# Kernel tuning notes

Measured on AMD Instinct MI355X. Metric: run time of the kernel, lower is better.

The kernel has to match this reference:

```python
import jax, jax.numpy as jnp
import numpy as np

NUM_LAYERS = 3
N = 4096
DIM = 512
TOPK = 8
BIG = 1.0e9
EPS_COS = 1e-8
EPS_NORM = 1e-12
BN_EPS = 1e-5
LAM_K = 64.0
LAM_Z = 16.0
SIGMA_INTRA = 0.99
ALPHA = np.linspace(1.0, 1.2, NUM_LAYERS)
BETA = np.linspace(0.0, 0.0, NUM_LAYERS)


def setup_inputs() -> dict:
    key = jax.random.key(0)
    ks = jax.random.split(key, 6)
    feats = jax.random.normal(ks[0], (NUM_LAYERS, N, DIM), dtype=jnp.float32)
    labels = jax.random.randint(ks[1], (N,), 0, 64, dtype=jnp.int64)
    fc1_w = jax.random.normal(ks[2], (NUM_LAYERS, DIM, DIM), dtype=jnp.float32) * (1.0 / np.sqrt(DIM))
    fc2_w = jax.random.normal(ks[3], (NUM_LAYERS, DIM, DIM), dtype=jnp.float32) * (1.0 / np.sqrt(DIM))
    bn_gamma = jnp.ones((NUM_LAYERS, DIM), dtype=jnp.float32)
    bn_beta = jnp.zeros((NUM_LAYERS, DIM), dtype=jnp.float32)
    proj_w = jax.random.normal(ks[4], (768, DIM), dtype=jnp.float32) * (1.0 / np.sqrt(DIM))
    return {"feats": feats, "labels": labels, "fc1_w": fc1_w, "fc2_w": fc2_w,
            "bn_gamma": bn_gamma, "bn_beta": bn_beta, "proj_w": proj_w}


def _l2norm(x, axis=-1):
    return x / jnp.maximum(jnp.linalg.norm(x, axis=axis, keepdims=True), EPS_NORM)


def _pairwise_cosine(G):
    Gn = _l2norm(G)
    sim = Gn @ Gn.T
    return jnp.clip(sim, -1.0 + EPS_COS, 1.0 - EPS_COS)


def _knn_mask(sim, base_mask, topk):
    n = sim.shape[0]
    masked = (sim - BIG * jnp.eye(n, dtype=sim.dtype)) * base_mask - (1.0 - base_mask) * BIG
    k = min(topk, max(n - 1, 1))
    idx = jax.lax.top_k(masked, k)[1]  # [N, k]
    st = jnp.zeros_like(sim).at[jnp.arange(n)[:, None], idx].set(1.0)
    return jnp.maximum(st, st.T)


def _build_intra_inter(sim, labels, topk):
    same = (labels[None, :] == labels[:, None]).astype(sim.dtype)
    diff = 1.0 - same
    m_intra = _knn_mask(sim, same, topk)
    m_inter = _knn_mask(sim, diff, topk)
    sim_intra = jnp.maximum(sim * m_intra, 0.0)
    sim_inter = jnp.maximum(sim * m_inter, 0.0)
    return sim_intra, sim_inter


def _normalize_sym(sim_graph, eps=1e-8):
    d = jnp.maximum(sim_graph.sum(axis=1), eps)
    dinv = d ** -0.5
    return dinv[:, None] * sim_graph * dinv[None, :]  # == diag(dinv) @ S @ diag(dinv)


def _diffusion(K, t_diff=1):
    out = K
    for _ in range(max(t_diff - 1, 0)):
        out = out @ K
    return out


def _bn_train(x, gamma, beta):
    m = x.mean(axis=0)
    v = x.var(axis=0)  # biased, as torch BN training
    return (x - m) / jnp.sqrt(v + BN_EPS) * gamma + beta


def _gam(S, G, w1, w2, gamma, beta):
    Z = S @ (G @ w1.T)
    Z = jax.nn.relu(_bn_train(Z, gamma, beta))
    Z = S @ (Z @ w2.T)
    return Z + G


def reference(feats, labels, fc1_w, fc2_w, bn_gamma, bn_beta, proj_w):
    n = feats.shape[1]
    eye = jnp.eye(n, dtype=feats.dtype)
    same = (labels[None, :] == labels[:, None]).astype(feats.dtype)

    K_list, Z_list = [], []
    for i in range(NUM_LAYERS):
        G = feats[i]
        sim = _pairwise_cosine(G)
        sim_intra, sim_inter = _build_intra_inter(sim, labels, TOPK)
        sim_graph = float(ALPHA[i]) * sim_intra + float(BETA[i]) * sim_inter + 1e-6 * eye
        S = _normalize_sym(sim_graph)
        K = _diffusion(S, t_diff=1)
        Z = _gam(S, G, fc1_w[i], fc2_w[i], bn_gamma[i], bn_beta[i])
        K_list.append(K)
        Z_list.append(Z)

    loss_K = jnp.zeros((), dtype=feats.dtype)
    loss_Z = jnp.zeros((), dtype=feats.dtype)
    for i in range(1, NUM_LAYERS):
        K_tgt = jax.lax.stop_gradient(K_list[i])
        loss_K = loss_K + jnp.mean((K_list[i - 1] - K_tgt) ** 2)
        Zp = _l2norm(Z_list[i - 1] @ proj_w.T)
        Zc = _l2norm(Z_list[i] @ proj_w.T)
        loss_Z = loss_Z + jnp.mean((Zp - jax.lax.stop_gradient(Zc)) ** 2)

    K_idea = _diffusion(same * SIGMA_INTRA, t_diff=1)
    loss_idea = jnp.mean((K_list[-1] - K_idea) ** 2)
    return LAM_K * loss_K + LAM_Z * loss_Z + loss_idea
```

## Files before the change

### kernel.cpp

```cpp
#include <hip/hip_runtime.h>
#include <math.h>
#include <stdint.h>

#define NROWS 4096
#define DIM   512
#define NCLS  64
#define CAP   128
#define PD    768
#define NL    3
#define PARTSZ (size_t)(NCLS * 4 * 1024)

typedef __attribute__((ext_vector_type(8))) short short8v;
typedef __attribute__((ext_vector_type(4))) float f32x4;

__device__ __forceinline__ unsigned short f2bf(float f) {
  unsigned u = __float_as_uint(f);
  unsigned r = (u + 0x7FFF + ((u >> 16) & 1)) >> 16;
  return (unsigned short)r;
}

__device__ __forceinline__ void gload_lds16(const void* g, void* l) {
  auto* lp = reinterpret_cast<__attribute__((address_space(3))) unsigned int*>(
      reinterpret_cast<uintptr_t>(l));
  const auto* gp = reinterpret_cast<const __attribute__((address_space(1))) unsigned int*>(
      reinterpret_cast<uintptr_t>(g));
  __builtin_amdgcn_global_load_lds(gp, lp, 16, 0, 0);
}

__device__ __forceinline__ float waveReduce(float v) {
#pragma unroll
  for (int o = 32; o > 0; o >>= 1) v += __shfl_down(v, o);
  return v;
}

__device__ __forceinline__ float blockReduce(float v) {
  __shared__ float sh[4];
  int lane = threadIdx.x & 63, wv = threadIdx.x >> 6;
  v = waveReduce(v);
  if (lane == 0) sh[wv] = v;
  __syncthreads();
  float t = 0.f;
  if (threadIdx.x == 0) {
    int nw = (blockDim.x + 63) >> 6;
    for (int i = 0; i < nw; ++i) t += sh[i];
  }
  return t;
}

__global__ __launch_bounds__(256) void k_hist(const int* __restrict__ labels, int* __restrict__ chunkCnt) {
  __shared__ int h[NCLS];
  int t = threadIdx.x;
  if (t < NCLS) h[t] = 0;
  __syncthreads();
  atomicAdd(&h[labels[blockIdx.x * 256 + t]], 1);
  __syncthreads();
  if (t < NCLS) chunkCnt[blockIdx.x * NCLS + t] = h[t];
}

__global__ void k_scan(const int* __restrict__ chunkCnt, int* __restrict__ cnt,
                       int* __restrict__ off, int* __restrict__ chunkBase, float* __restrict__ acc) {
  __shared__ int sc[NCLS];
  int c = threadIdx.x;
  if (c < 8) acc[c] = 0.f;
  int tot = 0;
  for (int b = 0; b < 16; ++b) tot += chunkCnt[b * NCLS + c];
  cnt[c] = tot;
  sc[c] = tot;
  __syncthreads();
  if (c == 0) {
    int s = 0;
    for (int i = 0; i < NCLS; ++i) { int tv = sc[i]; sc[i] = s; s += tv; }
  }
  __syncthreads();
  int run = sc[c];
  off[c] = run;
  for (int b = 0; b < 16; ++b) { chunkBase[b * NCLS + c] = run; run += chunkCnt[b * NCLS + c]; }
  if (c == 0) off[NCLS] = NROWS;
}

__global__ __launch_bounds__(256) void k_scatter(const int* __restrict__ labels, const int* __restrict__ chunkBase,
                                                 int* __restrict__ perm, int* __restrict__ clsp) {
  __shared__ int lab[256];
  int t = threadIdx.x;
  int r = blockIdx.x * 256 + t;
  int c = labels[r];
  lab[t] = c;
  __syncthreads();
  int rank = 0;
  for (int j = 0; j < t; ++j) rank += (lab[j] == c);
  int pos = chunkBase[blockIdx.x * NCLS + c] + rank;
  perm[pos] = r;
  clsp[pos] = c;
}

__global__ __launch_bounds__(128) void k_prepw(const float* __restrict__ feats, const int* __restrict__ perm,
                                               unsigned short* __restrict__ Gpb, float* __restrict__ invn,
                                               const float4* __restrict__ fc1, const float4* __restrict__ fc2,
                                               const float4* __restrict__ proj,
                                               ushort4* __restrict__ w1, ushort4* __restrict__ w2,
                                               ushort4* __restrict__ pj) {
  int y = blockIdx.y;
  if (y == NL) {
    const int nW = NL * DIM * DIM / 4;
    const int nP = PD * DIM / 4;
    int idx = blockIdx.x * 128 + threadIdx.x;
    const float4* src; ushort4* dst; int k;
    if (idx < nW) { src = fc1; dst = w1; k = idx; }
    else if (idx < 2 * nW) { src = fc2; dst = w2; k = idx - nW; }
    else if (idx < 2 * nW + nP) { src = proj; dst = pj; k = idx - 2 * nW; }
    else return;
    float4 v = src[k];
    ushort4 o;
    o.x = f2bf(v.x); o.y = f2bf(v.y); o.z = f2bf(v.z); o.w = f2bf(v.w);
    dst[k] = o;
    return;
  }
  __shared__ float red[2];
  int l = y;
  const float* G = feats + (size_t)l * NROWS * DIM;
  unsigned short* Gp = Gpb + (size_t)l * NROWS * DIM;
  int row = blockIdx.x, t = threadIdx.x;
  const float4* src = (const float4*)(G + (size_t)perm[row] * DIM);
  float4 v = src[t];
  ushort4 b;
  b.x = f2bf(v.x); b.y = f2bf(v.y); b.z = f2bf(v.z); b.w = f2bf(v.w);
  *(ushort4*)(Gp + (size_t)row * DIM + t * 4) = b;
  float ss = v.x * v.x + v.y * v.y + v.z * v.z + v.w * v.w;
  ss = waveReduce(ss);
  if ((t & 63) == 0) red[t >> 6] = ss;
  __syncthreads();
  if (t == 0) invn[l * NROWS + row] = 1.f / fmaxf(sqrtf(red[0] + red[1]), 1e-12f);
}

__global__ __launch_bounds__(256) void k_sim(const unsigned short* __restrict__ Gpb,
                                             const float* __restrict__ invn,
                                             const int* __restrict__ cnt, const int* __restrict__ off,
                                             float* __restrict__ sim) {
  int l = blockIdx.z;
  const unsigned short* Gp = Gpb + (size_t)l * NROWS * DIM;
  const float* inv = invn + (size_t)l * NROWS;
  float* sm = sim + (size_t)l * NCLS * CAP * CAP;
  int c = blockIdx.y;
  int n = min(cnt[c], CAP);
  int ti = blockIdx.x >> 2, tj = blockIdx.x & 3;
  if (ti * 32 >= n || tj * 32 >= n) return;
  int base = off[c];
  __shared__ short As[32][40];
  __shared__ short Bs[32][40];
  const int t = threadIdx.x;
  const int lane = t & 63, wv = t >> 6;
  const int qi = wv >> 1, qj = wv & 1;
  const int fr = lane & 15, kg = lane >> 4;
  const int half = t >> 7, tt = t & 127;
  const int srow = tt >> 2, scol = (tt & 3) * 8;
  int gr = (half ? tj : ti) * 32 + srow;
  const unsigned short* ps = Gp + (size_t)(base + min(gr, n - 1)) * DIM + scol;
  short* dst = half ? &Bs[srow][scol] : &As[srow][scol];
  f32x4 acc = {};
  for (int k0 = 0; k0 < DIM; k0 += 32) {
    short8v v = *(const short8v*)(ps + k0);
    __syncthreads();
    *(short8v*)dst = v;
    __syncthreads();
    short8v af = *(const short8v*)&As[qi * 16 + fr][kg * 8];
    short8v bf = *(const short8v*)&Bs[qj * 16 + fr][kg * 8];
    acc = __builtin_amdgcn_mfma_f32_16x16x32_bf16(af, bf, acc, 0, 0, 0);
  }
  int gj = tj * 32 + qj * 16 + fr;
  int r0 = ti * 32 + qi * 16 + kg * 4;
  if (gj < n) {
    float sj = inv[base + gj];
#pragma unroll
    for (int r = 0; r < 4; ++r) {
      int gi = r0 + r;
      if (gi < n) {
        float v = acc[r] * inv[base + gi] * sj;
        v = fminf(fmaxf(v, -1.0f + 1e-8f), 1.0f - 1e-8f);
        sm[((size_t)c * CAP + gi) * CAP + gj] = v;
      }
    }
  }
}

__global__ __launch_bounds__(256) void k_topk(const float* __restrict__ sim, const int* __restrict__ cnt,
                                              const int* __restrict__ off, const int* __restrict__ clsp,
                                              int* __restrict__ t8) {
  int l = blockIdx.y;
  const float* sm = sim + (size_t)l * NCLS * CAP * CAP;
  int* t8l = t8 + (size_t)l * NROWS * 8;
  int pr = blockIdx.x * 256 + threadIdx.x;
  if (pr >= NROWS) return;
  int c = clsp[pr];
  int n = min(cnt[c], CAP);
  int loc = pr - off[c];
  const float4* row4 = (const float4*)(sm + ((size_t)c * CAP + loc) * CAP);
  float bv[8]; int bi[8];
#pragma unroll
  for (int q = 0; q < 8; ++q) { bv[q] = -3e38f; bi[q] = -1; }
  for (int j4 = 0; j4 < CAP / 4; ++j4) {
    if (j4 * 4 >= n) break;
    float4 v4 = row4[j4];
    float vv[4] = {v4.x, v4.y, v4.z, v4.w};
#pragma unroll
    for (int k = 0; k < 4; ++k) {
      int j = j4 * 4 + k;
      if (j >= n || j == loc) continue;
      float v = vv[k];
      if (v > bv[7]) {
        bv[7] = v; bi[7] = j;
#pragma unroll
        for (int q = 7; q > 0; --q) {
          if (bv[q] > bv[q - 1]) {
            float tv = bv[q]; bv[q] = bv[q - 1]; bv[q - 1] = tv;
            int tq = bi[q]; bi[q] = bi[q - 1]; bi[q - 1] = tq;
          }
        }
      }
    }
  }
#pragma unroll
  for (int q = 0; q < 8; ++q) t8l[pr * 8 + q] = bi[q];
}

__global__ __launch_bounds__(256) void k_buildS1(const float* __restrict__ sim, const int* __restrict__ cnt,
                                                 const int* __restrict__ off, const int* __restrict__ t8,
                                                 float* __restrict__ S, float* __restrict__ dinv) {
  int l = blockIdx.z;
  float alpha = 1.0f + 0.1f * l;
  const float* sm = sim + (size_t)l * NCLS * CAP * CAP;
  float* Sl = S + (size_t)l * NCLS * CAP * CAP;
  const int* t8l = t8 + (size_t)l * NROWS * 8;
  float* dv = dinv + (size_t)l * NCLS * CAP;
  int c = blockIdx.x;
  int n = min(cnt[c], CAP);
  int i0 = blockIdx.y * 32;
  if (i0 >= n) return;
  int base = off[c];
  __shared__ int sh8[CAP * 8];
  for (int i = threadIdx.x; i < n * 8; i += 256) sh8[i] = t8l[base * 8 + i];
  __syncthreads();
  int r = threadIdx.x >> 3;
  int lj = threadIdx.x & 7;
  int i = i0 + r;
  float d = 0.f;
  if (i < n) {
    int my8[8];
#pragma unroll
    for (int q = 0; q < 8; ++q) my8[q] = sh8[i * 8 + q];
    const float* srow = sm + ((size_t)c * CAP + i) * CAP;
    float* wrow = Sl + ((size_t)c * CAP + i) * CAP;
    for (int j = lj; j < n; j += 8) {
      float w;
      if (j == i) w = 1e-6f;
      else {
        bool m = false;
#pragma unroll
        for (int q = 0; q < 8; ++q) m = m || (my8[q] == j) || (sh8[j * 8 + q] == i);
        w = m ? alpha * fmaxf(srow[j], 0.f) : 0.f;
      }
      wrow[j] = w;
      d += w;
    }
  }
  d += __shfl_xor(d, 1);
  d += __shfl_xor(d, 2);
  d += __shfl_xor(d, 4);
  if (lj == 0 && i < n) dv[c * CAP + i] = 1.f / sqrtf(fmaxf(d, 1e-8f));
}

__global__ __launch_bounds__(256) void k_buildS2(float* __restrict__ S, const float* __restrict__ dinv,
                                                 const int* __restrict__ cnt) {
  int l = blockIdx.z;
  float* Sl = S + (size_t)l * NCLS * CAP * CAP;
  const float* dv = dinv + (size_t)l * NCLS * CAP;
  int c = blockIdx.x;
  int n = min(cnt[c], CAP);
  int i0 = blockIdx.y * 32;
  if (i0 >= n) return;
  __shared__ float sd[CAP];
  for (int k = threadIdx.x; k < n; k += 256) sd[k] = dv[c * CAP + k];
  __syncthreads();
  for (int p = threadIdx.x; p < 32 * CAP; p += 256) {
    int r = p >> 7, j = p & (CAP - 1);
    int i = i0 + r;
    if (i < n && j < n)
      Sl[((size_t)c * CAP + i) * CAP + j] *= sd[i] * sd[j];
  }
}

__global__ __launch_bounds__(256) void k_gemm_bf16(const short* __restrict__ A, const short* __restrict__ B,
                                                   float* __restrict__ C, int N,
                                                   long sA, long sB, long sC) {
  int l = blockIdx.z;
  A += (size_t)l * sA; B += (size_t)l * sB; C += (size_t)l * sC;
  __shared__ __align__(16) short As[128][32];
  __shared__ __align__(16) short Bs[64][32];
  const int row0 = blockIdx.x * 128, col0 = blockIdx.y * 64;
  const int t = threadIdx.x;
  const int lane = t & 63, wv = t >> 6;
  const int fr = lane & 15, kg = lane >> 4;
  const int srow = lane >> 2, skb = (lane & 3) * 8;
  const short* pa = A + (size_t)(row0 + wv * 32 + srow) * DIM + skb;
  const short* pb = B + (size_t)(col0 + wv * 16 + srow) * DIM + skb;
  f32x4 acc[2][4] = {};
  for (int kt = 0; kt < DIM; kt += 32) {
    __syncthreads();
    gload_lds16(pa + kt, &As[wv * 32][0]);
    gload_lds16(pa + kt + (size_t)16 * DIM, &As[wv * 32 + 16][0]);
    gload_lds16(pb + kt, &Bs[wv * 16][0]);
    __syncthreads();
    short8v af[2], bf[4];
#pragma unroll
    for (int i = 0; i < 2; ++i) af[i] = *(const short8v*)&As[wv * 32 + i * 16 + fr][kg * 8];
#pragma unroll
    for (int j = 0; j < 4; ++j) bf[j] = *(const short8v*)&Bs[j * 16 + fr][kg * 8];
#pragma unroll
    for (int i = 0; i < 2; ++i)
#pragma unroll
      for (int j = 0; j < 4; ++j)
        acc[i][j] = __builtin_amdgcn_mfma_f32_16x16x32_bf16(af[i], bf[j], acc[i][j], 0, 0, 0);
  }
#pragma unroll
  for (int i = 0; i < 2; ++i) {
    int r0 = row0 + wv * 32 + i * 16 + kg * 4;
#pragma unroll
    for (int j = 0; j < 4; ++j) {
      int cc = col0 + j * 16 + fr;
#pragma unroll
      for (int r = 0; r < 4; ++r)
        C[(size_t)(r0 + r) * N + cc] = acc[i][j][r];
    }
  }
}

__global__ __launch_bounds__(256) void k_spmm4(const float* __restrict__ S, const float* __restrict__ X,
                                               const float* __restrict__ Gfeat, const int* __restrict__ perm,
                                               float* __restrict__ Y, unsigned short* __restrict__ Yb,
                                               float* __restrict__ part,
                                               const int* __restrict__ cnt, const int* __restrict__ off) {
  int l = blockIdx.z >> 2;
  int zc = blockIdx.z & 3;
  const float* Sl = S + (size_t)l * NCLS * CAP * CAP;
  const float4* X4 = (const float4*)(X + (size_t)l * NROWS * DIM);
  const float4* G4 = Gfeat ? (const float4*)(Gfeat + (size_t)l * NROWS * DIM) : (const float4*)nullptr;
  float4* Y4 = Y ? (float4*)(Y + (size_t)l * NROWS * DIM) : (float4*)nullptr;
  ushort4* Yb4 = Yb ? (ushort4*)(Yb + (size_t)l * NROWS * DIM) : (ushort4*)nullptr;
  int c = blockIdx.x;
  int n = min(cnt[c], CAP);
  int i0 = zc * 32;
  float* pslot = part ? part + (size_t)l * PARTSZ + (size_t)(c * 4 + zc) * 1024 : (float*)nullptr;
  __shared__ float sS[32][CAP];
  if (i0 >= n) {
    if (pslot) {
      int col = blockIdx.y * 256 + threadIdx.x;
      pslot[col] = 0.f;
      pslot[512 + col] = 0.f;
    }
    return;
  }
  int base = off[c];
  int lane = threadIdx.x & 63;
  int col4 = blockIdx.y * 64 + lane;
  int ty = threadIdx.x >> 6;
  for (int idx = threadIdx.x; idx < 32 * n; idx += 256) {
    int r = idx / n, j = idx - r * n;
    sS[r][j] = (i0 + r < n) ? Sl[((size_t)c * CAP + i0 + r) * CAP + j] : 0.f;
  }
  __syncthreads();
  float4 acc[8];
#pragma unroll
  for (int ii = 0; ii < 8; ++ii) acc[ii] = make_float4(0.f, 0.f, 0.f, 0.f);
  for (int j = 0; j < n; ++j) {
    float4 x = X4[(size_t)(base + j) * 128 + col4];
#pragma unroll
    for (int ii = 0; ii < 8; ++ii) {
      float s = sS[ty * 8 + ii][j];
      acc[ii].x += s * x.x;
      acc[ii].y += s * x.y;
      acc[ii].z += s * x.z;
      acc[ii].w += s * x.w;
    }
  }
  float s1[4] = {0.f, 0.f, 0.f, 0.f}, s2[4] = {0.f, 0.f, 0.f, 0.f};
#pragma unroll
  for (int ii = 0; ii < 8; ++ii) {
    int r = i0 + ty * 8 + ii;
    if (r < n) {
      size_t o = (size_t)(base + r) * 128 + col4;
      float4 v = acc[ii];
      if (G4) {
        float4 g = G4[(size_t)perm[base + r] * 128 + col4];
        v.x += g.x; v.y += g.y; v.z += g.z; v.w += g.w;
      }
      if (pslot) {
        s1[0] += v.x; s1[1] += v.y; s1[2] += v.z; s1[3] += v.w;
        s2[0] += v.x * v.x; s2[1] += v.y * v.y; s2[2] += v.z * v.z; s2[3] += v.w * v.w;
      }
      if (Yb4) {
        ushort4 ob;
        ob.x = f2bf(v.x); ob.y = f2bf(v.y); ob.z = f2bf(v.z); ob.w = f2bf(v.w);
        Yb4[o] = ob;
      } else {
        Y4[o] = v;
      }
    }
  }
  if (pslot) {
    __syncthreads();
    float* scr = &sS[0][0];
#pragma unroll
    for (int q = 0; q < 4; ++q) {
      scr[(ty * 64 + lane) * 8 + q] = s1[q];
      scr[(ty * 64 + lane) * 8 + 4 + q] = s2[q];
    }
    __syncthreads();
    if (ty == 0) {
#pragma unroll
      for (int q = 0; q < 4; ++q) {
        float a = 0.f, b = 0.f;
#pragma unroll
        for (int g = 0; g < 4; ++g) {
          a += scr[(g * 64 + lane) * 8 + q];
          b += scr[(g * 64 + lane) * 8 + 4 + q];
        }
        int col = blockIdx.y * 256 + lane * 4 + q;
        pslot[col] = a;
        pslot[512 + col] = b;
      }
    }
  }
}

__global__ __launch_bounds__(64) void k_bnfin(const float* __restrict__ part, const float* __restrict__ gamma,
                                              const float* __restrict__ beta, float* __restrict__ sc) {
  int l = blockIdx.y;
  const float* pl = part + (size_t)l * PARTSZ;
  int k = blockIdx.x * 64 + threadIdx.x;
  float s = 0.f, s2 = 0.f;
  for (int b = 0; b < NCLS * 4; ++b) {
    s += pl[b * 1024 + k];
    s2 += pl[b * 1024 + 512 + k];
  }
  float m = s * (1.f / NROWS);
  float var = s2 * (1.f / NROWS) - m * m;
  float sg = gamma[l * DIM + k] / sqrtf(var + 1e-5f);
  sc[l * 2 * DIM + k] = sg;
  sc[l * 2 * DIM + DIM + k] = beta[l * DIM + k] - m * sg;
}

__global__ __launch_bounds__(256) void k_bnrelu(const float4* __restrict__ X, const float* __restrict__ sc,
                                                ushort4* __restrict__ Yb) {
  int l = blockIdx.y;
  const float4* Xl = X + (size_t)l * (NROWS * DIM / 4);
  const float* scl = sc + (size_t)l * 2 * DIM;
  ushort4* Yl = Yb + (size_t)l * (NROWS * DIM / 4);
  int i = blockIdx.x * blockDim.x + threadIdx.x;
  int cb = (i * 4) & (DIM - 1);
  float4 v = Xl[i];
  ushort4 o;
  o.x = f2bf(fmaxf(v.x * scl[cb + 0] + scl[DIM + cb + 0], 0.f));
  o.y = f2bf(fmaxf(v.y * scl[cb + 1] + scl[DIM + cb + 1], 0.f));
  o.z = f2bf(fmaxf(v.z * scl[cb + 2] + scl[DIM + cb + 2], 0.f));
  o.w = f2bf(fmaxf(v.w * scl[cb + 3] + scl[DIM + cb + 3], 0.f));
  Yl[i] = o;
}

__global__ __launch_bounds__(192) void k_rownormP(float* __restrict__ P) {
  __shared__ float red[3];
  __shared__ float s_inv;
  int l = blockIdx.y;
  float* Pl = P + (size_t)l * NROWS * PD;
  int row = blockIdx.x, t = threadIdx.x;
  float4* p = (float4*)(Pl + (size_t)row * PD);
  float4 v = p[t];
  float ss = v.x * v.x + v.y * v.y + v.z * v.z + v.w * v.w;
  ss = waveReduce(ss);
  if ((t & 63) == 0) red[t >> 6] = ss;
  __syncthreads();
  if (t == 0) s_inv = 1.f / fmaxf(sqrtf(red[0] + red[1] + red[2]), 1e-12f);
  __syncthreads();
  float inv = s_inv;
  v.x *= inv; v.y *= inv; v.z *= inv; v.w *= inv;
  p[t] = v;
}

__global__ __launch_bounds__(256) void k_loss(const float* __restrict__ S, const float* __restrict__ P,
                                              const int* __restrict__ cnt,
                                              float target, float cK, float cI, float cZ,
                                              float* __restrict__ acc) {
  int y = blockIdx.y;
  if (y < 3) {
    if (blockIdx.x >= NCLS) return;
    const float* Sa = S + (size_t)y * NCLS * CAP * CAP;
    const float* Sb = nullptr;
    float coef;
    if (y < 2) { Sb = Sa + (size_t)NCLS * CAP * CAP; coef = cK; }
    else { Sa = S + (size_t)2 * NCLS * CAP * CAP; coef = cI; }
    int c = blockIdx.x;
    int n = min(cnt[c], CAP);
    float s = 0.f;
    for (int p = threadIdx.x; p < CAP * CAP; p += 256) {
      int i = p >> 7, j = p & (CAP - 1);
      if (i < n && j < n) {
        size_t o = ((size_t)c * CAP + i) * CAP + j;
        float d = Sb ? (Sa[o] - Sb[o]) : (Sa[o] - target);
        s += d * d;
      }
    }
    s = blockReduce(s);
    if (threadIdx.x == 0) atomicAdd(acc, s * coef);
  } else {
    int yy = y - 3;
    const float* A = P + (size_t)yy * NROWS * PD;
    const float* B = A + (size_t)NROWS * PD;
    const int nel = NROWS * PD;
    float s = 0.f;
    for (int i = blockIdx.x * blockDim.x + threadIdx.x; i < nel; i += gridDim.x * blockDim.x) {
      float d = A[i] - B[i];
      s += d * d;
    }
    s = blockReduce(s);
    if (threadIdx.x == 0) atomicAdd(acc, s * cZ);
  }
}

__global__ void k_final(const float* __restrict__ acc, float* __restrict__ out) {
  if (threadIdx.x == 0) out[0] = acc[0];
}

extern "C" void kernel_launch(void* const* d_in, const int* in_sizes, int n_in,
                              void* d_out, int out_size, void* d_ws, size_t ws_size,
                              hipStream_t stream) {
  const float* feats = (const float*)d_in[0];
  const int* labels = (const int*)d_in[1];
  const float* fc1 = (const float*)d_in[2];
  const float* fc2 = (const float*)d_in[3];
  const float* gamma = (const float*)d_in[4];
  const float* beta = (const float*)d_in[5];
  const float* proj = (const float*)d_in[6];
  float* out = (float*)d_out;

  char* w = (char*)d_ws;
  auto alloc = [&](size_t bytes) { char* p = w; w += (bytes + 255) & ~(size_t)255; return p; };
  float* bufA = (float*)alloc((size_t)NL * NROWS * DIM * 4);
  float* bufB = (float*)alloc((size_t)NL * NROWS * DIM * 4);
  unsigned short* Gpb = (unsigned short*)alloc((size_t)NL * NROWS * DIM * 2);
  unsigned short* actb = (unsigned short*)alloc((size_t)NL * NROWS * DIM * 2);
  unsigned short* W1b = (unsigned short*)alloc((size_t)NL * DIM * DIM * 2);
  unsigned short* W2b = (unsigned short*)alloc((size_t)NL * DIM * DIM * 2);
  unsigned short* Pjb = (unsigned short*)alloc((size_t)PD * DIM * 2);
  float* sim  = (float*)alloc((size_t)NL * NCLS * CAP * CAP * 4);
  float* S    = (float*)alloc((size_t)NL * NCLS * CAP * CAP * 4);
  float* P    = (float*)alloc((size_t)NL * NROWS * PD * 4);
  float* invn = (float*)alloc((size_t)NL * NROWS * 4);
  float* dinv = (float*)alloc((size_t)NL * NCLS * CAP * 4);
  float* part = (float*)alloc((size_t)NL * PARTSZ * 4);
  float* bnsc = (float*)alloc((size_t)NL * 2 * DIM * 4);
  float* acc  = (float*)alloc(256);
  int* cnt  = (int*)alloc(NCLS * 4);
  int* offc = (int*)alloc((NCLS + 1) * 4);
  int* perm = (int*)alloc(NROWS * 4);
  int* clsp = (int*)alloc(NROWS * 4);
  int* t8   = (int*)alloc((size_t)NL * NROWS * 8 * 4);
  int* chunkCnt  = (int*)alloc(16 * NCLS * 4);
  int* chunkBase = (int*)alloc(16 * NCLS * 4);

  const float LAM_K = 64.f, LAM_Z = 16.f, SIGMA = 0.99f;
  const float cK = LAM_K / ((float)NROWS * (float)NROWS);
  const float cZ = LAM_Z / ((float)NROWS * (float)PD);
  const float cI = 1.f / ((float)NROWS * (float)NROWS);
  const long sAct = (long)NROWS * DIM;
  const long sW = (long)DIM * DIM;

  hipLaunchKernelGGL(k_hist, dim3(16), dim3(256), 0, stream, labels, chunkCnt);
  hipLaunchKernelGGL(k_scan, dim3(1), dim3(64), 0, stream, chunkCnt, cnt, offc, chunkBase, acc);
  hipLaunchKernelGGL(k_scatter, dim3(16), dim3(256), 0, stream, labels, chunkBase, perm, clsp);

  hipLaunchKernelGGL(k_prepw, dim3(NROWS, NL + 1), dim3(128), 0, stream, feats, perm, Gpb, invn,
                     (const float4*)fc1, (const float4*)fc2, (const float4*)proj,
                     (ushort4*)W1b, (ushort4*)W2b, (ushort4*)Pjb);

  hipLaunchKernelGGL(k_sim, dim3(16, NCLS, NL), dim3(256), 0, stream, Gpb, invn, cnt, offc, sim);
  hipLaunchKernelGGL(k_topk, dim3(NROWS / 256, NL), dim3(256), 0, stream, sim, cnt, offc, clsp, t8);
  hipLaunchKernelGGL(k_buildS1, dim3(NCLS, CAP / 32, NL), dim3(256), 0, stream, sim, cnt, offc, t8, S, dinv);
  hipLaunchKernelGGL(k_buildS2, dim3(NCLS, CAP / 32, NL), dim3(256), 0, stream, S, dinv, cnt);

  hipLaunchKernelGGL(k_gemm_bf16, dim3(NROWS / 128, DIM / 64, NL), dim3(256), 0, stream,
                     (const short*)Gpb, (const short*)W1b, bufA, DIM, sAct, sW, (long)NROWS * DIM);
  hipLaunchKernelGGL(k_spmm4, dim3(NCLS, DIM / 256, 4 * NL), dim3(256), 0, stream, S, bufA,
                     (const float*)nullptr, (const int*)nullptr, bufB, (unsigned short*)nullptr, part, cnt, offc);
  hipLaunchKernelGGL(k_bnfin, dim3(DIM / 64, NL), dim3(64), 0, stream, part, gamma, beta, bnsc);
  hipLaunchKernelGGL(k_bnrelu, dim3(NROWS * DIM / 4 / 256, NL), dim3(256), 0, stream,
                     (const float4*)bufB, bnsc, (ushort4*)actb);
  hipLaunchKernelGGL(k_gemm_bf16, dim3(NROWS / 128, DIM / 64, NL), dim3(256), 0, stream,
                     (const short*)actb, (const short*)W2b, bufB, DIM, sAct, sW, (long)NROWS * DIM);
  hipLaunchKernelGGL(k_spmm4, dim3(NCLS, DIM / 256, 4 * NL), dim3(256), 0, stream, S, bufB,
                     feats, perm, (float*)nullptr, actb, (float*)nullptr, cnt, offc);
  hipLaunchKernelGGL(k_gemm_bf16, dim3(NROWS / 128, PD / 64, NL), dim3(256), 0, stream,
                     (const short*)actb, (const short*)Pjb, P, PD, sAct, 0L, (long)NROWS * PD);
  hipLaunchKernelGGL(k_rownormP, dim3(NROWS, NL), dim3(192), 0, stream, P);

  hipLaunchKernelGGL(k_loss, dim3(512, 5), dim3(256), 0, stream, S, P, cnt, SIGMA, cK, cI, cZ, acc);

  hipLaunchKernelGGL(k_final, dim3(1), dim3(64), 0, stream, acc, out);
}
```

Measured before the change: 265.2 us.

## Fuse projection row norms into GEMM epilogue and widen SpMM row tiles

The projection GEMM epilogue now accumulates per-row sums of squares with shuffles and atomics into a buffer zeroed in the prep kernel. That removes the separate row-normalization pass over P, and the loss kernel applies the inverse norms on the fly. Separately, the SpMM kernel now handles 64 rows per block instead of 32, halving the number of blocks and BN partial slots. The cost is more register pressure (16 float4 accumulators), a larger shared-memory tile, less parallelism, and atomic contention on the row-norm buffer.

New measurement: 262.9 us. Within noise of the previous version (-0.9%).

```diff
diff --git a/kernel.cpp b/kernel.cpp
--- a/kernel.cpp
+++ b/kernel.cpp
@@ -8,7 +8,7 @@
 #define CAP   128
 #define PD    768
 #define NL    3
-#define PARTSZ (size_t)(NCLS * 4 * 1024)
+#define PARTSZ (size_t)(NCLS * 2 * 1024)
 
 typedef __attribute__((ext_vector_type(8))) short short8v;
 typedef __attribute__((ext_vector_type(4))) float f32x4;
@@ -98,7 +98,7 @@
                                                const float4* __restrict__ fc1, const float4* __restrict__ fc2,
                                                const float4* __restrict__ proj,
                                                ushort4* __restrict__ w1, ushort4* __restrict__ w2,
-                                               ushort4* __restrict__ pj) {
+                                               ushort4* __restrict__ pj, float* __restrict__ rnorm) {
   int y = blockIdx.y;
   if (y == NL) {
     const int nW = NL * DIM * DIM / 4;
@@ -108,7 +108,11 @@
     if (idx < nW) { src = fc1; dst = w1; k = idx; }
     else if (idx < 2 * nW) { src = fc2; dst = w2; k = idx - nW; }
     else if (idx < 2 * nW + nP) { src = proj; dst = pj; k = idx - 2 * nW; }
-    else return;
+    else {
+      int z = idx - (2 * nW + nP);
+      if (z < NL * NROWS) rnorm[z] = 0.f;
+      return;
+    }
     float4 v = src[k];
     ushort4 o;
     o.x = f2bf(v.x); o.y = f2bf(v.y); o.z = f2bf(v.z); o.w = f2bf(v.w);
@@ -289,10 +293,11 @@
 }
 
 __global__ __launch_bounds__(256) void k_gemm_bf16(const short* __restrict__ A, const short* __restrict__ B,
-                                                   float* __restrict__ C, int N,
+                                                   float* __restrict__ C, float* __restrict__ rnorm, int N,
                                                    long sA, long sB, long sC) {
   int l = blockIdx.z;
   A += (size_t)l * sA; B += (size_t)l * sB; C += (size_t)l * sC;
+  if (rnorm) rnorm += (size_t)l * NROWS;
   __shared__ __align__(16) short As[128][32];
   __shared__ __align__(16) short Bs[64][32];
   const int row0 = blockIdx.x * 128, col0 = blockIdx.y * 64;
@@ -330,16 +335,28 @@
       for (int r = 0; r < 4; ++r)
         C[(size_t)(r0 + r) * N + cc] = acc[i][j][r];
     }
-  }
-}
-
-__global__ __launch_bounds__(256) void k_spmm4(const float* __restrict__ S, const float* __restrict__ X,
-                                               const float* __restrict__ Gfeat, const int* __restrict__ perm,
-                                               float* __restrict__ Y, unsigned short* __restrict__ Yb,
-                                               float* __restrict__ part,
-                                               const int* __restrict__ cnt, const int* __restrict__ off) {
-  int l = blockIdx.z >> 2;
-  int zc = blockIdx.z & 3;
+    if (rnorm) {
+#pragma unroll
+      for (int r = 0; r < 4; ++r) {
+        float ss = acc[i][0][r] * acc[i][0][r] + acc[i][1][r] * acc[i][1][r] +
+                   acc[i][2][r] * acc[i][2][r] + acc[i][3][r] * acc[i][3][r];
+        ss += __shfl_xor(ss, 1);
+        ss += __shfl_xor(ss, 2);
+        ss += __shfl_xor(ss, 4);
+        ss += __shfl_xor(ss, 8);
+        if (fr == 0) atomicAdd(&rnorm[r0 + r], ss);
+      }
+    }
+  }
+}
+
+__global__ __launch_bounds__(256) void k_spmm64(const float* __restrict__ S, const float* __restrict__ X,
+                                                const float* __restrict__ Gfeat, const int* __restrict__ perm,
+                                                float* __restrict__ Y, unsigned short* __restrict__ Yb,
+                                                float* __restrict__ part,
+                                                const int* __restrict__ cnt, const int* __restrict__ off) {
+  int l = blockIdx.z >> 1;
+  int zc = blockIdx.z & 1;
   const float* Sl = S + (size_t)l * NCLS * CAP * CAP;
   const float4* X4 = (const float4*)(X + (size_t)l * NROWS * DIM);
   const float4* G4 = Gfeat ? (const float4*)(Gfeat + (size_t)l * NROWS * DIM) : (const float4*)nullptr;
@@ -347,9 +364,9 @@
   ushort4* Yb4 = Yb ? (ushort4*)(Yb + (size_t)l * NROWS * DIM) : (ushort4*)nullptr;
   int c = blockIdx.x;
   int n = min(cnt[c], CAP);
-  int i0 = zc * 32;
-  float* pslot = part ? part + (size_t)l * PARTSZ + (size_t)(c * 4 + zc) * 1024 : (float*)nullptr;
-  __shared__ float sS[32][CAP];
+  int i0 = zc * 64;
+  float* pslot = part ? part + (size_t)l * PARTSZ + (size_t)(c * 2 + zc) * 1024 : (float*)nullptr;
+  __shared__ float sS[64][CAP];
   if (i0 >= n) {
     if (pslot) {
       int col = blockIdx.y * 256 + threadIdx.x;
@@ -362,19 +379,19 @@
   int lane = threadIdx.x & 63;
   int col4 = blockIdx.y * 64 + lane;
   int ty = threadIdx.x >> 6;
-  for (int idx = threadIdx.x; idx < 32 * n; idx += 256) {
+  for (int idx = threadIdx.x; idx < 64 * n; idx += 256) {
     int r = idx / n, j = idx - r * n;
     sS[r][j] = (i0 + r < n) ? Sl[((size_t)c * CAP + i0 + r) * CAP + j] : 0.f;
   }
   __syncthreads();
-  float4 acc[8];
-#pragma unroll
-  for (int ii = 0; ii < 8; ++ii) acc[ii] = make_float4(0.f, 0.f, 0.f, 0.f);
+  float4 acc[16];
+#pragma unroll
+  for (int ii = 0; ii < 16; ++ii) acc[ii] = make_float4(0.f, 0.f, 0.f, 0.f);
   for (int j = 0; j < n; ++j) {
     float4 x = X4[(size_t)(base + j) * 128 + col4];
 #pragma unroll
-    for (int ii = 0; ii < 8; ++ii) {
-      float s = sS[ty * 8 + ii][j];
+    for (int ii = 0; ii < 16; ++ii) {
+      float s = sS[ty * 16 + ii][j];
       acc[ii].x += s * x.x;
       acc[ii].y += s * x.y;
       acc[ii].z += s * x.z;
@@ -383,8 +400,8 @@
   }
   float s1[4] = {0.f, 0.f, 0.f, 0.f}, s2[4] = {0.f, 0.f, 0.f, 0.f};
 #pragma unroll
-  for (int ii = 0; ii < 8; ++ii) {
-    int r = i0 + ty * 8 + ii;
+  for (int ii = 0; ii < 16; ++ii) {
+    int r = i0 + ty * 16 + ii;
     if (r < n) {
       size_t o = (size_t)(base + r) * 128 + col4;
       float4 v = acc[ii];
@@ -437,7 +454,7 @@
   const float* pl = part + (size_t)l * PARTSZ;
   int k = blockIdx.x * 64 + threadIdx.x;
   float s = 0.f, s2 = 0.f;
-  for (int b = 0; b < NCLS * 4; ++b) {
+  for (int b = 0; b < NCLS * 2; ++b) {
     s += pl[b * 1024 + k];
     s2 += pl[b * 1024 + 512 + k];
   }
@@ -465,27 +482,8 @@
   Yl[i] = o;
 }
 
-__global__ __launch_bounds__(192) void k_rownormP(float* __restrict__ P) {
-  __shared__ float red[3];
-  __shared__ float s_inv;
-  int l = blockIdx.y;
-  float* Pl = P + (size_t)l * NROWS * PD;
-  int row = blockIdx.x, t = threadIdx.x;
-  float4* p = (float4*)(Pl + (size_t)row * PD);
-  float4 v = p[t];
-  float ss = v.x * v.x + v.y * v.y + v.z * v.z + v.w * v.w;
-  ss = waveReduce(ss);
-  if ((t & 63) == 0) red[t >> 6] = ss;
-  __syncthreads();
-  if (t == 0) s_inv = 1.f / fmaxf(sqrtf(red[0] + red[1] + red[2]), 1e-12f);
-  __syncthreads();
-  float inv = s_inv;
-  v.x *= inv; v.y *= inv; v.z *= inv; v.w *= inv;
-  p[t] = v;
-}
-
 __global__ __launch_bounds__(256) void k_loss(const float* __restrict__ S, const float* __restrict__ P,
-                                              const int* __restrict__ cnt,
+                                              const float* __restrict__ rnorm, const int* __restrict__ cnt,
                                               float target, float cK, float cI, float cZ,
                                               float* __restrict__ acc) {
   int y = blockIdx.y;
@@ -513,11 +511,21 @@
     int yy = y - 3;
     const float* A = P + (size_t)yy * NROWS * PD;
     const float* B = A + (size_t)NROWS * PD;
-    const int nel = NROWS * PD;
+    const float* rnA = rnorm + (size_t)yy * NROWS;
+    const float* rnB = rnA + NROWS;
     float s = 0.f;
-    for (int i = blockIdx.x * blockDim.x + threadIdx.x; i < nel; i += gridDim.x * blockDim.x) {
-      float d = A[i] - B[i];
-      s += d * d;
+    int row0 = blockIdx.x * 8;
+#pragma unroll
+    for (int ii = 0; ii < 8; ++ii) {
+      int row = row0 + ii;
+      float ia = 1.f / fmaxf(sqrtf(rnA[row]), 1e-12f);
+      float ib = 1.f / fmaxf(sqrtf(rnB[row]), 1e-12f);
+      const float* pa = A + (size_t)row * PD;
+      const float* pb = B + (size_t)row * PD;
+      for (int cidx = threadIdx.x; cidx < PD; cidx += 256) {
+        float d = pa[cidx] * ia - pb[cidx] * ib;
+        s += d * d;
+      }
     }
     s = blockReduce(s);
     if (threadIdx.x == 0) atomicAdd(acc, s * cZ);
@@ -556,6 +564,7 @@
   float* dinv = (float*)alloc((size_t)NL * NCLS * CAP * 4);
   float* part = (float*)alloc((size_t)NL * PARTSZ * 4);
   float* bnsc = (float*)alloc((size_t)NL * 2 * DIM * 4);
+  float* rnorm = (float*)alloc((size_t)NL * NROWS * 4);
   float* acc  = (float*)alloc(256);
   int* cnt  = (int*)alloc(NCLS * 4);
   int* offc = (int*)alloc((NCLS + 1) * 4);
@@ -578,7 +587,7 @@
 
   hipLaunchKernelGGL(k_prepw, dim3(NROWS, NL + 1), dim3(128), 0, stream, feats, perm, Gpb, invn,
                      (const float4*)fc1, (const float4*)fc2, (const float4*)proj,
-                     (ushort4*)W1b, (ushort4*)W2b, (ushort4*)Pjb);
+                     (ushort4*)W1b, (ushort4*)W2b, (ushort4*)Pjb, rnorm);
 
   hipLaunchKernelGGL(k_sim, dim3(16, NCLS, NL), dim3(256), 0, stream, Gpb, invn, cnt, offc, sim);
   hipLaunchKernelGGL(k_topk, dim3(NROWS / 256, NL), dim3(256), 0, stream, sim, cnt, offc, clsp, t8);
@@ -586,21 +595,20 @@
   hipLaunchKernelGGL(k_buildS2, dim3(NCLS, CAP / 32, NL), dim3(256), 0, stream, S, dinv, cnt);
 
   hipLaunchKernelGGL(k_gemm_bf16, dim3(NROWS / 128, DIM / 64, NL), dim3(256), 0, stream,
-                     (const short*)Gpb, (const short*)W1b, bufA, DIM, sAct, sW, (long)NROWS * DIM);
-  hipLaunchKernelGGL(k_spmm4, dim3(NCLS, DIM / 256, 4 * NL), dim3(256), 0, stream, S, bufA,
+                     (const short*)Gpb, (const short*)W1b, bufA, (float*)nullptr, DIM, sAct, sW, (long)NROWS * DIM);
+  hipLaunchKernelGGL(k_spmm64, dim3(NCLS, DIM / 256, 2 * NL), dim3(256), 0, stream, S, bufA,
                      (const float*)nullptr, (const int*)nullptr, bufB, (unsigned short*)nullptr, part, cnt, offc);
   hipLaunchKernelGGL(k_bnfin, dim3(DIM / 64, NL), dim3(64), 0, stream, part, gamma, beta, bnsc);
   hipLaunchKernelGGL(k_bnrelu, dim3(NROWS * DIM / 4 / 256, NL), dim3(256), 0, stream,
                      (const float4*)bufB, bnsc, (ushort4*)actb);
   hipLaunchKernelGGL(k_gemm_bf16, dim3(NROWS / 128, DIM / 64, NL), dim3(256), 0, stream,
-                     (const short*)actb, (const short*)W2b, bufB, DIM, sAct, sW, (long)NROWS * DIM);
-  hipLaunchKernelGGL(k_spmm4, dim3(NCLS, DIM / 256, 4 * NL), dim3(256), 0, stream, S, bufB,
+                     (const short*)actb, (const short*)W2b, bufB, (float*)nullptr, DIM, sAct, sW, (long)NROWS * DIM);
+  hipLaunchKernelGGL(k_spmm64, dim3(NCLS, DIM / 256, 2 * NL), dim3(256), 0, stream, S, bufB,
                      feats, perm, (float*)nullptr, actb, (float*)nullptr, cnt, offc);
   hipLaunchKernelGGL(k_gemm_bf16, dim3(NROWS / 128, PD / 64, NL), dim3(256), 0, stream,
-                     (const short*)actb, (const short*)Pjb, P, PD, sAct, 0L, (long)NROWS * PD);
-  hipLaunchKernelGGL(k_rownormP, dim3(NROWS, NL), dim3(192), 0, stream, P);
-
-  hipLaunchKernelGGL(k_loss, dim3(512, 5), dim3(256), 0, stream, S, P, cnt, SIGMA, cK, cI, cZ, acc);
+                     (const short*)actb, (const short*)Pjb, P, rnorm, PD, sAct, 0L, (long)NROWS * PD);
+
+  hipLaunchKernelGGL(k_loss, dim3(512, 5), dim3(256), 0, stream, S, P, rnorm, cnt, SIGMA, cK, cI, cZ, acc);
 
   hipLaunchKernelGGL(k_final, dim3(1), dim3(64), 0, stream, acc, out);
 }
```
